# Kernel tuning notes

Measured on AMD Instinct MI355X. Metric: run time of the kernel, lower is better.

Reference implementation:

```python
import jax, jax.numpy as jnp
import numpy as np
from jax import lax

EPS = 1e-5
NBIT = 127.0  # 8-bit symmetric: 2^(8-1)-1

def ste_round(x):
    return x + lax.stop_gradient(jnp.round(x) - x)

def quant_act(x, rng_max):
    # symmetric fake-quant of activations with learned per-cluster range
    s = rng_max / NBIT
    xq = jnp.clip(ste_round(x / s), -NBIT, NBIT) * s
    return xq, s

def fold_bn(w, gamma, beta, mean, var):
    std = jnp.sqrt(var + EPS)
    scale = gamma / std
    w_f = w * scale[:, None, None, None]
    b_f = beta - mean * scale
    return w_f, b_f

def quant_weight(w):
    # per-output-channel symmetric quant
    s = jnp.max(jnp.abs(w), axis=(1, 2, 3), keepdims=True) / NBIT
    wq = jnp.clip(ste_round(w / s), -NBIT, NBIT) * s
    return wq, s.reshape(-1)

def conv(x, w, stride=1, groups=1, pad=0):
    return lax.conv_general_dilated(
        x, w, window_strides=(stride, stride),
        padding=((pad, pad), (pad, pad)),
        dimension_numbers=('NCHW', 'OIHW', 'NCHW'),
        feature_group_count=groups)

def setup_inputs() -> dict:
    key = jax.random.key(0)
    ks = jax.random.split(key, 24)
    B, Cin, H, W = 64, 96, 28, 28
    Cmid, Cout, NC = 576, 96, 4
    d = {}
    d['x'] = jax.random.normal(ks[0], (B, Cin, H, W), dtype=jnp.float32)
    # conv1: 1x1 expansion
    d['w1'] = jax.random.normal(ks[1], (Cmid, Cin, 1, 1), jnp.float32) * 0.1
    d['g1'] = jax.random.uniform(ks[2], (Cmid,), minval=0.5, maxval=1.5)
    d['b1'] = jax.random.normal(ks[3], (Cmid,)) * 0.1
    d['m1'] = jax.random.normal(ks[4], (Cmid,)) * 0.1
    d['v1'] = jax.random.uniform(ks[5], (Cmid,), minval=0.5, maxval=1.5)
    # conv2: 3x3 depthwise
    d['w2'] = jax.random.normal(ks[6], (Cmid, 1, 3, 3), jnp.float32) * 0.1
    d['g2'] = jax.random.uniform(ks[7], (Cmid,), minval=0.5, maxval=1.5)
    d['b2'] = jax.random.normal(ks[8], (Cmid,)) * 0.1
    d['m2'] = jax.random.normal(ks[9], (Cmid,)) * 0.1
    d['v2'] = jax.random.uniform(ks[10], (Cmid,), minval=0.5, maxval=1.5)
    # conv3: 1x1 projection
    d['w3'] = jax.random.normal(ks[11], (Cout, Cmid, 1, 1), jnp.float32) * 0.1
    d['g3'] = jax.random.uniform(ks[12], (Cout,), minval=0.5, maxval=1.5)
    d['b3'] = jax.random.normal(ks[13], (Cout,)) * 0.1
    d['m3'] = jax.random.normal(ks[14], (Cout,)) * 0.1
    d['v3'] = jax.random.uniform(ks[15], (Cout,), minval=0.5, maxval=1.5)
    # per-cluster learned activation ranges for the 4 QuantAct modules
    d['r0'] = jax.random.uniform(ks[16], (NC,), minval=2.0, maxval=8.0)
    d['r1'] = jax.random.uniform(ks[17], (NC,), minval=2.0, maxval=8.0)
    d['r2'] = jax.random.uniform(ks[18], (NC,), minval=2.0, maxval=8.0)
    d['r3'] = jax.random.uniform(ks[19], (NC,), minval=2.0, maxval=8.0)
    d['cluster'] = 2
    return d

def reference(x, w1, g1, b1, m1, v1, w2, g2, b2, m2, v2,
              w3, g3, b3, m3, v3, r0, r1, r2, r3, cluster):
    identity = x  # residual path (in==out, stride==1)
    # QuantAct -> conv1 (BN-folded, per-channel quant) -> ReLU6
    xq, s0 = quant_act(x, r0[cluster])
    w1f, bf1 = fold_bn(w1, g1, b1, m1, v1)
    w1q, ws1 = quant_weight(w1f)
    y = conv(xq, w1q) + bf1[None, :, None, None]
    y = jnp.clip(y, 0.0, 6.0)
    # QuantAct1 -> depthwise conv2 -> ReLU6
    yq, s1 = quant_act(y, r1[cluster])
    w2f, bf2 = fold_bn(w2, g2, b2, m2, v2)
    w2q, ws2 = quant_weight(w2f)
    y = conv(yq, w2q, stride=1, groups=w2.shape[0], pad=1) + bf2[None, :, None, None]
    y = jnp.clip(y, 0.0, 6.0)
    # QuantAct2 -> conv3 projection
    yq, s2 = quant_act(y, r2[cluster])
    w3f, bf3 = fold_bn(w3, g3, b3, m3, v3)
    w3q, ws3 = quant_weight(w3f)
    y = conv(yq, w3q) + bf3[None, :, None, None]
    # residual add, then int32 requant
    y = y + identity
    out, s3 = quant_act(y, r3[cluster])
    return out, s3
```

## Files before the change

kernel.cpp:

```cpp
#include <hip/hip_runtime.h>
#include <cstdint>
#include <cstddef>

typedef int   v4i __attribute__((ext_vector_type(4)));
typedef float v4f __attribute__((ext_vector_type(4)));
typedef unsigned int u32;

constexpr int B_   = 64;
constexpr int CIN  = 96;
constexpr int P_   = 784;
constexpr int CMID = 576;
constexpr int COUT = 96;
constexpr int NOUT = B_ * COUT * P_;
constexpr float NBITF = 127.0f;
constexpr float EPSF  = 1e-5f;

constexpr int XKD = 36;
constexpr int YKD = 144;
constexpr int XBD = 13 * XKD * 64;
constexpr int YBD = 13 * YKD * 64;

__device__ __forceinline__ int dot3(u32 a, u32 w, int acc) {
#if __has_builtin(__builtin_amdgcn_sdot4)
    return __builtin_amdgcn_sdot4((int)a, (int)w, acc, false);
#else
    return acc + (int)(signed char)(a)        * (int)(signed char)(w)
               + (int)(signed char)(a >> 8)   * (int)(signed char)(w >> 8)
               + (int)(signed char)(a >> 16)  * (int)(signed char)(w >> 16);
#endif
}

__device__ __forceinline__ void tr4(u32 S0, u32 S1, u32 S2, u32 S3, u32 O[4]) {
    u32 u01 = __builtin_amdgcn_perm(S1, S0, 0x05010400u);
    u32 u23 = __builtin_amdgcn_perm(S3, S2, 0x05010400u);
    u32 v01 = __builtin_amdgcn_perm(S1, S0, 0x07030602u);
    u32 v23 = __builtin_amdgcn_perm(S3, S2, 0x07030602u);
    O[0] = __builtin_amdgcn_perm(u23, u01, 0x05040100u);
    O[1] = __builtin_amdgcn_perm(u23, u01, 0x07060302u);
    O[2] = __builtin_amdgcn_perm(v23, v01, 0x05040100u);
    O[3] = __builtin_amdgcn_perm(v23, v01, 0x07060302u);
}

__global__ __launch_bounds__(64)
void prep_weights(const float* __restrict__ w1, const float* __restrict__ g1,
                  const float* __restrict__ b1, const float* __restrict__ m1,
                  const float* __restrict__ v1,
                  const float* __restrict__ w2, const float* __restrict__ g2,
                  const float* __restrict__ b2, const float* __restrict__ m2,
                  const float* __restrict__ v2,
                  const float* __restrict__ w3, const float* __restrict__ g3,
                  const float* __restrict__ b3, const float* __restrict__ m3,
                  const float* __restrict__ v3,
                  int8_t* __restrict__ w1qp, float* __restrict__ ws1, float* __restrict__ bf1,
                  v4i* __restrict__ w2pk, float* __restrict__ ws2, float* __restrict__ bf2,
                  int8_t* __restrict__ w3qp, float* __restrict__ ws3, float* __restrict__ bf3)
{
    int blk  = blockIdx.x;
    int lane = threadIdx.x;

    const float *w, *g, *bb, *mm, *vv;
    int oc, K, which;
    if (blk < CMID)            { which = 0; w = w1; g = g1; bb = b1; mm = m1; vv = v1; oc = blk;            K = CIN;  }
    else if (blk < 2 * CMID)   { which = 1; w = w2; g = g2; bb = b2; mm = m2; vv = v2; oc = blk - CMID;     K = 9;    }
    else                       { which = 2; w = w3; g = g3; bb = b3; mm = m3; vv = v3; oc = blk - 2 * CMID; K = CMID; }

    float scale = g[oc] / sqrtf(vv[oc] + EPSF);

    float mx = 0.f;
    for (int k = lane; k < K; k += 64)
        mx = fmaxf(mx, fabsf(w[oc * K + k] * scale));
    #pragma unroll
    for (int off = 1; off < 64; off <<= 1)
        mx = fmaxf(mx, __shfl_xor(mx, off));

    float s = mx / NBITF;

    int myq = 0;
    for (int k = lane; k < K; k += 64) {
        float wf = w[oc * K + k] * scale;
        float q  = fminf(fmaxf(rintf(wf / s), -127.f), 127.f);
        if (which == 0)      w1qp[oc * 144 + k] = (int8_t)q;
        else if (which == 1) myq = (int)q;
        else                 w3qp[oc * 592 + k] = (int8_t)q;
    }
    if (which == 0 && lane < 12)
        ((u32*)(w1qp + oc * 144))[24 + lane] = 0u;
    if (which == 1) {
        u32 qq[9];
        #pragma unroll
        for (int t = 0; t < 9; t++) qq[t] = (u32)__shfl(myq, t, 64) & 0xffu;
        if (lane == 0) {
            v4i pk;
            pk[0] = (int)(qq[0] | (qq[1] << 8) | (qq[2] << 16));
            pk[1] = (int)(qq[3] | (qq[4] << 8) | (qq[5] << 16));
            pk[2] = (int)(qq[6] | (qq[7] << 8) | (qq[8] << 16));
            pk[3] = 0;
            w2pk[oc] = pk;
        }
    }
    if (lane == 0) {
        float bf = bb[oc] - mm[oc] * scale;
        if (which == 0)      { ws1[oc] = s; bf1[oc] = bf; }
        else if (which == 1) { ws2[oc] = s; bf2[oc] = bf; }
        else                 { ws3[oc] = s; bf3[oc] = bf; }
    }
}

__global__ __launch_bounds__(256)
void quant_x(const float* __restrict__ x, const float* __restrict__ r0,
             const int* __restrict__ cluster, u32* __restrict__ x8t)
{
    __shared__ u32 T[112 * 37];

    int tid = threadIdx.x, pt0 = blockIdx.x, b = blockIdx.y;
    float inv_s0 = NBITF / r0[cluster[0]];

    for (int i = tid; i < 112 * 12; i += 256) {
        int row = i / 12, cpad = i - row * 12;
        T[row * 37 + 24 + cpad] = 0u;
    }
    for (int u = tid; u < 24 * 28; u += 256) {
        int pq = u % 28, icq = u / 28;
        int pxb = pt0 * 112 + pq * 4;
        int q[4][4];
        #pragma unroll
        for (int j = 0; j < 4; j++) {
            v4f xv = *(const v4f*)(x + ((size_t)b * CIN + icq * 4 + j) * P_ + pxb);
            #pragma unroll
            for (int i = 0; i < 4; i++)
                q[j][i] = (int)fminf(fmaxf(rintf(xv[i] * inv_s0), -127.f), 127.f);
        }
        #pragma unroll
        for (int i = 0; i < 4; i++) {
            u32 t0 = __builtin_amdgcn_perm((u32)q[1][i], (u32)q[0][i], 0x00000400u);
            u32 t1 = __builtin_amdgcn_perm((u32)q[3][i], (u32)q[2][i], 0x00000400u);
            T[(pq * 4 + i) * 37 + icq] = __builtin_amdgcn_perm(t1, t0, 0x05040100u);
        }
    }
    __syncthreads();
    u32* gb = x8t + (size_t)b * XBD;
    for (int i = tid; i < XKD * 112; i += 256) {
        int icq = i / 112, pxo = i - icq * 112;
        int px = pt0 * 112 + pxo;
        gb[(((px >> 6) * XKD) + icq) * 64 + (px & 63)] = T[pxo * 37 + icq];
    }
}

__global__ __launch_bounds__(256)
void conv12(const u32* __restrict__ x8t, const int8_t* __restrict__ w1qp,
            const float* __restrict__ ws1, const float* __restrict__ bf1,
            const v4i* __restrict__ w2pk, const float* __restrict__ ws2,
            const float* __restrict__ bf2,
            const float* __restrict__ r0, const float* __restrict__ r1,
            const float* __restrict__ r2, const int* __restrict__ cluster,
            u32* __restrict__ y2qT)
{
    __shared__ u32 AY[6912];
    __shared__ u32 PB[5488];

    int tid = threadIdx.x;
    int b   = blockIdx.y;
    int mt  = blockIdx.x / 14, rt = blockIdx.x - mt * 14;
    int oc0 = mt * 192;
    int R0  = rt * 2;
    int W0  = (R0 - 1) * 28;

    int   c      = cluster[0];
    float s0     = r0[c] / NBITF;
    float s1     = r1[c] / NBITF;
    float inv_s1 = NBITF / r1[c];
    float inv_s2 = NBITF / r2[c];
    float u1     = fminf(rintf(6.f * inv_s1), 127.f);
    float u2     = fminf(rintf(6.f * inv_s2), 127.f);

    {
        const v4i* gs = (const v4i*)(w1qp + (size_t)oc0 * 144);
        v4i* ld = (v4i*)AY;
        for (int i = tid; i < 192 * 9; i += 256) ld[i] = gs[i];
    }
    __syncthreads();

    int lane = tid & 63, wv = tid >> 6;
    int n = lane & 15, q4 = lane >> 4;

    const u32* xb = x8t + (size_t)b * XBD;
    int pbase[7];
    #pragma unroll
    for (int j = 0; j < 7; j++) {
        int px = W0 + j * 16 + n;
        px = min(max(px, 0), P_ - 1);
        pbase[j] = ((px >> 6) * XKD) * 64 + (px & 63);
    }

    v4i acc[3][7];
    #pragma unroll
    for (int i = 0; i < 3; i++)
        #pragma unroll
        for (int j = 0; j < 7; j++) acc[i][j] = (v4i){0, 0, 0, 0};

    const v4i* Af = (const v4i*)AY;
    #pragma unroll
    for (int ks = 0; ks < 2; ks++) {
        int k0 = ks * 16 + q4 * 4;
        v4i bfr[7], afr[3];
        #pragma unroll
        for (int j = 0; j < 7; j++) {
            u32 d0 = xb[pbase[j] + (k0 + 0) * 64];
            u32 d1 = xb[pbase[j] + (k0 + 1) * 64];
            u32 d2 = xb[pbase[j] + (k0 + 2) * 64];
            u32 d3 = xb[pbase[j] + (k0 + 3) * 64];
            bfr[j] = (v4i){(int)d0, (int)d1, (int)d2, (int)d3};
        }
        #pragma unroll
        for (int i = 0; i < 3; i++)
            afr[i] = Af[(wv * 48 + i * 16 + n) * 9 + ks * 4 + q4];
        #pragma unroll
        for (int i = 0; i < 3; i++)
            #pragma unroll
            for (int j = 0; j < 7; j++)
                acc[i][j] = __builtin_amdgcn_mfma_i32_16x16x64_i8(afr[i], bfr[j], acc[i][j], 0, 0, 0);
    }

    float sA[3][4], bA[3][4];
    #pragma unroll
    for (int i = 0; i < 3; i++)
        #pragma unroll
        for (int r = 0; r < 4; r++) {
            int oc = oc0 + wv * 48 + i * 16 + q4 * 4 + r;
            sA[i][r] = s0 * ws1[oc] * inv_s1;
            bA[i][r] = bf1[oc] * inv_s1;
        }
    #pragma unroll
    for (int i = 0; i < 3; i++) {
        int chq = wv * 12 + i * 4 + q4;
        #pragma unroll
        for (int j = 0; j < 7; j++) {
            int pxl = j * 16 + n;
            bool valid = (unsigned)(W0 + pxl) < (unsigned)P_;
            u32 pk = 0;
            #pragma unroll
            for (int r = 0; r < 4; r++) {
                float t = fmaf((float)acc[i][j][r], sA[i][r], bA[i][r]);
                t = fminf(fmaxf(rintf(t), 0.f), u1);
                pk |= ((u32)(int)t) << (8 * r);
            }
            PB[pxl * 49 + chq] = valid ? pk : 0u;
        }
    }
    __syncthreads();

    for (int u = tid; u < 1536; u += 256) {
        int cc = u & 7, rowl = (u >> 3) & 3, chq = u >> 5;
        u32 S[4];
        #pragma unroll
        for (int k = 0; k < 4; k++) {
            int col = 4 * cc - 1 + k;
            S[k] = ((unsigned)col < 28u) ? PB[(rowl * 28 + col) * 49 + chq] : 0u;
        }
        u32 O[4];
        tr4(S[0], S[1], S[2], S[3], O);
        int bse = chq * 132 + rowl * 8 + cc;
        #pragma unroll
        for (int r = 0; r < 4; r++) AY[bse + r * 33] = O[r];
    }
    __syncthreads();

    for (int u = tid; u < 2688; u += 256) {
        int xq = u % 7;
        int t2 = u / 7;
        int orow = t2 & 1;
        int chl  = t2 >> 1;
        int chg  = oc0 + chl;

        v4i wpk = w2pk[chg];
        int base = chl * 33 + orow * 8;
        int a0 = 0, a1 = 0, a2 = 0, a3 = 0;
        #pragma unroll
        for (int dr = 0; dr < 3; dr++) {
            u32 d0 = AY[base + dr * 8 + xq];
            u32 d1 = AY[base + dr * 8 + xq + 1];
            u32 pk = (u32)((dr == 0) ? wpk[0] : (dr == 1) ? wpk[1] : wpk[2]);
            a0 = dot3(d0, pk, a0);
            a1 = dot3(__builtin_amdgcn_alignbyte(d1, d0, 1), pk, a1);
            a2 = dot3(__builtin_amdgcn_alignbyte(d1, d0, 2), pk, a2);
            a3 = dot3(__builtin_amdgcn_alignbyte(d1, d0, 3), pk, a3);
        }
        float sc = s1 * ws2[chg] * inv_s2;
        float bb = bf2[chg] * inv_s2;
        int aa[4] = {a0, a1, a2, a3};
        u32 pk2 = 0;
        #pragma unroll
        for (int i = 0; i < 4; i++) {
            float t = fmaf((float)aa[i], sc, bb);
            t = fminf(fmaxf(rintf(t), 0.f), u2);
            pk2 |= ((u32)(int)t) << (8 * i);
        }
        PB[chl * 15 + orow * 7 + xq] = pk2;
    }
    __syncthreads();

    u32* yb = y2qT + (size_t)b * YBD;
    int kdw0 = mt * 48;
    for (int u = tid; u < 672; u += 256) {
        int pxq = u % 14, chq = u / 14;
        int orow = pxq / 7, xq = pxq - orow * 7;
        u32 S[4];
        #pragma unroll
        for (int r = 0; r < 4; r++) S[r] = PB[(chq * 4 + r) * 15 + pxq];
        u32 O[4];
        tr4(S[0], S[1], S[2], S[3], O);
        #pragma unroll
        for (int k = 0; k < 4; k++) {
            int gpx = (R0 + orow) * 28 + xq * 4 + k;
            yb[((gpx >> 6) * YKD + kdw0 + chq) * 64 + (gpx & 63)] = O[k];
        }
    }
}

__global__ __launch_bounds__(256)
void conv3_kernel(const u32* __restrict__ y2qT, const int8_t* __restrict__ w3qp,
                  const float* __restrict__ ws3, const float* __restrict__ bf3,
                  const float* __restrict__ x, const float* __restrict__ r2,
                  const float* __restrict__ r3, const int* __restrict__ cluster,
                  float* __restrict__ out)
{
    __shared__ u32 Ash[96 * 148];

    int tid = threadIdx.x, b = blockIdx.y, pt = blockIdx.x;

    int   c      = cluster[0];
    float s2     = r2[c] / NBITF;
    float s3     = r3[c] / NBITF;
    float inv_s3 = NBITF / r3[c];

    {
        const v4i* gs = (const v4i*)w3qp;
        v4i* ld = (v4i*)Ash;
        for (int i = tid; i < 96 * 37; i += 256) ld[i] = gs[i];
    }
    __syncthreads();

    int lane = tid & 63, wv = tid >> 6;
    int n = lane & 15, q4 = lane >> 4;
    int pxl = wv * 16 + n;

    const u32* yb = y2qT + (size_t)b * YBD + (size_t)pt * (YKD * 64) + pxl;
    const v4i* Af = (const v4i*)Ash;

    v4i acc[6];
    #pragma unroll
    for (int i = 0; i < 6; i++) acc[i] = (v4i){0, 0, 0, 0};

    #pragma unroll
    for (int ks = 0; ks < 9; ks++) {
        int k0 = ks * 16 + q4 * 4;
        u32 d0 = yb[(k0 + 0) * 64];
        u32 d1 = yb[(k0 + 1) * 64];
        u32 d2 = yb[(k0 + 2) * 64];
        u32 d3 = yb[(k0 + 3) * 64];
        v4i bfr = (v4i){(int)d0, (int)d1, (int)d2, (int)d3};
        #pragma unroll
        for (int i = 0; i < 6; i++) {
            v4i afr = Af[(i * 16 + n) * 37 + ks * 4 + q4];
            acc[i] = __builtin_amdgcn_mfma_i32_16x16x64_i8(afr, bfr, acc[i], 0, 0, 0);
        }
    }

    int px = pt * 64 + pxl;
    if (px < P_) {
        #pragma unroll
        for (int i = 0; i < 6; i++)
            #pragma unroll
            for (int r = 0; r < 4; r++) {
                int oc = i * 16 + q4 * 4 + r;
                size_t gi = ((size_t)b * COUT + oc) * P_ + px;
                float v  = (float)acc[i][r] * (s2 * ws3[oc]) + bf3[oc] + x[gi];
                float qv = fminf(fmaxf(rintf(v * inv_s3), -127.f), 127.f);
                out[gi] = qv * s3;
            }
    }
    if (pt == 0 && b == 0 && tid == 0)
        out[NOUT] = s3;
}

extern "C" void kernel_launch(void* const* d_in, const int* in_sizes, int n_in,
                              void* d_out, int out_size, void* d_ws, size_t ws_size,
                              hipStream_t stream)
{
    const float* x  = (const float*)d_in[0];
    const float* w1 = (const float*)d_in[1];
    const float* g1 = (const float*)d_in[2];
    const float* b1 = (const float*)d_in[3];
    const float* m1 = (const float*)d_in[4];
    const float* v1 = (const float*)d_in[5];
    const float* w2 = (const float*)d_in[6];
    const float* g2 = (const float*)d_in[7];
    const float* b2 = (const float*)d_in[8];
    const float* m2 = (const float*)d_in[9];
    const float* v2 = (const float*)d_in[10];
    const float* w3 = (const float*)d_in[11];
    const float* g3 = (const float*)d_in[12];
    const float* b3 = (const float*)d_in[13];
    const float* m3 = (const float*)d_in[14];
    const float* v3 = (const float*)d_in[15];
    const float* r0 = (const float*)d_in[16];
    const float* r1 = (const float*)d_in[17];
    const float* r2 = (const float*)d_in[18];
    const float* r3 = (const float*)d_in[19];
    const int*   cl = (const int*)d_in[20];

    float* out = (float*)d_out;

    char*  ws  = (char*)d_ws;
    size_t off = 0;
    auto carve = [&](size_t bytes) {
        size_t cur = off;
        off = (off + bytes + 255) & ~(size_t)255;
        return (void*)(ws + cur);
    };
    int8_t* w1qp = (int8_t*)carve((size_t)CMID * 144);
    float*  ws1  = (float*)carve(CMID * 4);
    float*  bf1  = (float*)carve(CMID * 4);
    v4i*    w2pk = (v4i*)carve((size_t)CMID * 16);
    float*  ws2  = (float*)carve(CMID * 4);
    float*  bf2  = (float*)carve(CMID * 4);
    int8_t* w3qp = (int8_t*)carve((size_t)COUT * 592);
    float*  ws3  = (float*)carve(COUT * 4);
    float*  bf3  = (float*)carve(COUT * 4);
    u32*    x8t  = (u32*)carve((size_t)B_ * XBD * 4);
    u32*    y2qT = (u32*)carve((size_t)B_ * YBD * 4);
    (void)ws_size; (void)in_sizes; (void)n_in; (void)out_size;

    prep_weights<<<dim3(2 * CMID + COUT), dim3(64), 0, stream>>>(
        w1, g1, b1, m1, v1, w2, g2, b2, m2, v2, w3, g3, b3, m3, v3,
        w1qp, ws1, bf1, w2pk, ws2, bf2, w3qp, ws3, bf3);

    quant_x<<<dim3(7, B_), dim3(256), 0, stream>>>(x, r0, cl, x8t);

    conv12<<<dim3(42, B_), dim3(256), 0, stream>>>(
        x8t, w1qp, ws1, bf1, w2pk, ws2, bf2, r0, r1, r2, cl, y2qT);

    conv3_kernel<<<dim3(13, B_), dim3(256), 0, stream>>>(
        y2qT, w3qp, ws3, bf3, x, r2, r3, cl, out);
}
```

Before: 191.0 us.

## Split fused conv1+depthwise kernel into separate conv1, depthwise, conv3 kernels

The fused conv1+depthwise kernel is split into three kernels: an MFMA 1x1 expansion that writes packed int8 rows in channel-major layout, a per-row depthwise kernel that reads them from global memory, and a projection kernel that transposes the activations into LDS instead of the weights. Rounding and clamping now use the magic-number float trick on integer bits. The change drops the halo recomputation and the shared-memory staging of the fused kernel. In exchange the full 576-channel intermediate makes an extra round trip through global memory, and the x8t buffer is aliased onto y2px.

After: 187.7 us. No clear change (-1.7%).

```diff
diff --git a/kernel.cpp b/kernel.cpp
--- a/kernel.cpp
+++ b/kernel.cpp
@@ -14,11 +14,11 @@
 constexpr int NOUT = B_ * COUT * P_;
 constexpr float NBITF = 127.0f;
 constexpr float EPSF  = 1e-5f;
+constexpr float MAGICF = 12582912.0f;
+constexpr int   BIASI  = 0x4B400000;
 
 constexpr int XKD = 36;
-constexpr int YKD = 144;
 constexpr int XBD = 13 * XKD * 64;
-constexpr int YBD = 13 * YKD * 64;
 
 __device__ __forceinline__ int dot3(u32 a, u32 w, int acc) {
 #if __has_builtin(__builtin_amdgcn_sdot4)
@@ -39,6 +39,12 @@
     O[1] = __builtin_amdgcn_perm(u23, u01, 0x07060302u);
     O[2] = __builtin_amdgcn_perm(v23, v01, 0x05040100u);
     O[3] = __builtin_amdgcn_perm(v23, v01, 0x07060302u);
+}
+
+__device__ __forceinline__ u32 pack4(u32 t0, u32 t1, u32 t2, u32 t3) {
+    u32 p01 = __builtin_amdgcn_perm(t1, t0, 0x05010400u);
+    u32 p23 = __builtin_amdgcn_perm(t3, t2, 0x05010400u);
+    return __builtin_amdgcn_perm(p23, p01, 0x05040100u);
 }
 
 __global__ __launch_bounds__(64)
@@ -147,196 +153,175 @@
 }
 
 __global__ __launch_bounds__(256)
-void conv12(const u32* __restrict__ x8t, const int8_t* __restrict__ w1qp,
+void conv1s(const u32* __restrict__ x8t, const int8_t* __restrict__ w1qp,
             const float* __restrict__ ws1, const float* __restrict__ bf1,
-            const v4i* __restrict__ w2pk, const float* __restrict__ ws2,
-            const float* __restrict__ bf2,
             const float* __restrict__ r0, const float* __restrict__ r1,
-            const float* __restrict__ r2, const int* __restrict__ cluster,
-            u32* __restrict__ y2qT)
-{
-    __shared__ u32 AY[6912];
-    __shared__ u32 PB[5488];
-
-    int tid = threadIdx.x;
-    int b   = blockIdx.y;
-    int mt  = blockIdx.x / 14, rt = blockIdx.x - mt * 14;
-    int oc0 = mt * 192;
-    int R0  = rt * 2;
-    int W0  = (R0 - 1) * 28;
+            const int* __restrict__ cluster, u32* __restrict__ y1px)
+{
+    int tid = threadIdx.x, b = blockIdx.y;
+    int mt = blockIdx.x % 3, pt = blockIdx.x / 3;
+    int p0 = pt * 64;
+    int lane = tid & 63, wv = tid >> 6;
+    int n = lane & 15, q4 = lane >> 4;
+    int ocw = mt * 192 + wv * 48;
 
     int   c      = cluster[0];
     float s0     = r0[c] / NBITF;
-    float s1     = r1[c] / NBITF;
     float inv_s1 = NBITF / r1[c];
-    float inv_s2 = NBITF / r2[c];
-    float u1     = fminf(rintf(6.f * inv_s1), 127.f);
-    float u2     = fminf(rintf(6.f * inv_s2), 127.f);
-
-    {
-        const v4i* gs = (const v4i*)(w1qp + (size_t)oc0 * 144);
-        v4i* ld = (v4i*)AY;
-        for (int i = tid; i < 192 * 9; i += 256) ld[i] = gs[i];
-    }
-    __syncthreads();
-
-    int lane = tid & 63, wv = tid >> 6;
-    int n = lane & 15, q4 = lane >> 4;
+    int   u1i    = (int)fminf(rintf(6.f * inv_s1), 127.f);
 
     const u32* xb = x8t + (size_t)b * XBD;
-    int pbase[7];
-    #pragma unroll
-    for (int j = 0; j < 7; j++) {
-        int px = W0 + j * 16 + n;
-        px = min(max(px, 0), P_ - 1);
-        pbase[j] = ((px >> 6) * XKD) * 64 + (px & 63);
-    }
-
-    v4i acc[3][7];
-    #pragma unroll
-    for (int i = 0; i < 3; i++)
-        #pragma unroll
-        for (int j = 0; j < 7; j++) acc[i][j] = (v4i){0, 0, 0, 0};
-
-    const v4i* Af = (const v4i*)AY;
+    int abase[4];
+    #pragma unroll
+    for (int jm = 0; jm < 4; jm++) {
+        int px = p0 + 16 * jm + n;
+        px = min(px, P_ - 1);
+        abase[jm] = ((px >> 6) * XKD) * 64 + (px & 63);
+    }
+
+    v4i acc[3][4];
+    #pragma unroll
+    for (int jn = 0; jn < 3; jn++)
+        #pragma unroll
+        for (int jm = 0; jm < 4; jm++) acc[jn][jm] = (v4i){0, 0, 0, 0};
+
+    const v4i* w4 = (const v4i*)w1qp;
     #pragma unroll
     for (int ks = 0; ks < 2; ks++) {
-        int k0 = ks * 16 + q4 * 4;
-        v4i bfr[7], afr[3];
-        #pragma unroll
-        for (int j = 0; j < 7; j++) {
-            u32 d0 = xb[pbase[j] + (k0 + 0) * 64];
-            u32 d1 = xb[pbase[j] + (k0 + 1) * 64];
-            u32 d2 = xb[pbase[j] + (k0 + 2) * 64];
-            u32 d3 = xb[pbase[j] + (k0 + 3) * 64];
-            bfr[j] = (v4i){(int)d0, (int)d1, (int)d2, (int)d3};
-        }
-        #pragma unroll
-        for (int i = 0; i < 3; i++)
-            afr[i] = Af[(wv * 48 + i * 16 + n) * 9 + ks * 4 + q4];
-        #pragma unroll
-        for (int i = 0; i < 3; i++)
+        v4i bfr[3], afr[4];
+        #pragma unroll
+        for (int jn = 0; jn < 3; jn++) {
+            int oc = ocw + 16 * jn + n;
+            bfr[jn] = w4[oc * 9 + ks * 4 + q4];
+        }
+        #pragma unroll
+        for (int jm = 0; jm < 4; jm++) {
+            int kb = (16 * ks + 4 * q4) * 64;
+            u32 d0 = xb[abase[jm] + kb];
+            u32 d1 = xb[abase[jm] + kb + 64];
+            u32 d2 = xb[abase[jm] + kb + 128];
+            u32 d3 = xb[abase[jm] + kb + 192];
+            afr[jm] = (v4i){(int)d0, (int)d1, (int)d2, (int)d3};
+        }
+        #pragma unroll
+        for (int jn = 0; jn < 3; jn++)
             #pragma unroll
-            for (int j = 0; j < 7; j++)
-                acc[i][j] = __builtin_amdgcn_mfma_i32_16x16x64_i8(afr[i], bfr[j], acc[i][j], 0, 0, 0);
-    }
-
-    float sA[3][4], bA[3][4];
-    #pragma unroll
-    for (int i = 0; i < 3; i++)
-        #pragma unroll
-        for (int r = 0; r < 4; r++) {
-            int oc = oc0 + wv * 48 + i * 16 + q4 * 4 + r;
-            sA[i][r] = s0 * ws1[oc] * inv_s1;
-            bA[i][r] = bf1[oc] * inv_s1;
-        }
-    #pragma unroll
-    for (int i = 0; i < 3; i++) {
-        int chq = wv * 12 + i * 4 + q4;
-        #pragma unroll
-        for (int j = 0; j < 7; j++) {
-            int pxl = j * 16 + n;
-            bool valid = (unsigned)(W0 + pxl) < (unsigned)P_;
-            u32 pk = 0;
+            for (int jm = 0; jm < 4; jm++)
+                acc[jn][jm] = __builtin_amdgcn_mfma_i32_16x16x64_i8(afr[jm], bfr[jn], acc[jn][jm], 0, 0, 0);
+    }
+
+    #pragma unroll
+    for (int jn = 0; jn < 3; jn++) {
+        int   oc  = ocw + 16 * jn + n;
+        float scv = s0 * ws1[oc] * inv_s1;
+        float bbv = bf1[oc] * inv_s1;
+        size_t rowbase = (size_t)(b * CMID + oc) * 196 + (p0 >> 2);
+        #pragma unroll
+        for (int jm = 0; jm < 4; jm++) {
+            int quad = p0 + 16 * jm + 4 * q4;
+            u32 t[4];
             #pragma unroll
             for (int r = 0; r < 4; r++) {
-                float t = fmaf((float)acc[i][j][r], sA[i][r], bA[i][r]);
-                t = fminf(fmaxf(rintf(t), 0.f), u1);
-                pk |= ((u32)(int)t) << (8 * r);
+                float f = fmaf((float)acc[jn][jm][r], scv, bbv) + MAGICF;
+                int v = __float_as_int(f);
+                t[r] = (u32)min(max(v, BIASI), BIASI + u1i);
             }
-            PB[pxl * 49 + chq] = valid ? pk : 0u;
-        }
-    }
-    __syncthreads();
-
-    for (int u = tid; u < 1536; u += 256) {
-        int cc = u & 7, rowl = (u >> 3) & 3, chq = u >> 5;
-        u32 S[4];
-        #pragma unroll
-        for (int k = 0; k < 4; k++) {
-            int col = 4 * cc - 1 + k;
-            S[k] = ((unsigned)col < 28u) ? PB[(rowl * 28 + col) * 49 + chq] : 0u;
-        }
-        u32 O[4];
-        tr4(S[0], S[1], S[2], S[3], O);
-        int bse = chq * 132 + rowl * 8 + cc;
-        #pragma unroll
-        for (int r = 0; r < 4; r++) AY[bse + r * 33] = O[r];
-    }
-    __syncthreads();
-
-    for (int u = tid; u < 2688; u += 256) {
-        int xq = u % 7;
-        int t2 = u / 7;
-        int orow = t2 & 1;
-        int chl  = t2 >> 1;
-        int chg  = oc0 + chl;
-
-        v4i wpk = w2pk[chg];
-        int base = chl * 33 + orow * 8;
+            if (quad < P_)
+                y1px[rowbase + 4 * jm + q4] = pack4(t[0], t[1], t[2], t[3]);
+        }
+    }
+}
+
+__global__ __launch_bounds__(256)
+void conv2s(const u32* __restrict__ y1px, const v4i* __restrict__ w2pk,
+            const float* __restrict__ ws2, const float* __restrict__ bf2,
+            const float* __restrict__ r1, const float* __restrict__ r2,
+            const int* __restrict__ cluster, u32* __restrict__ y2px)
+{
+    int gid = blockIdx.x * 256 + threadIdx.x;
+    int r  = gid % 28;
+    int t  = gid / 28;
+    int ch = t % CMID;
+    int b  = t / CMID;
+
+    int   c      = cluster[0];
+    float s1     = r1[c] / NBITF;
+    float inv_s2 = NBITF / r2[c];
+    int   u2i    = (int)fminf(rintf(6.f * inv_s2), 127.f);
+
+    const u32* base = y1px + (size_t)(b * CMID + ch) * 196;
+    u32 R[3][7];
+    #pragma unroll
+    for (int dr = 0; dr < 3; dr++) {
+        int rr = r + dr - 1;
+        bool ok = (unsigned)rr < 28u;
+        #pragma unroll
+        for (int j = 0; j < 7; j++)
+            R[dr][j] = ok ? base[rr * 7 + j] : 0u;
+    }
+
+    v4i wpk = w2pk[ch];
+    u32 pk0 = (u32)wpk[0], pk1 = (u32)wpk[1], pk2 = (u32)wpk[2];
+    float scv = s1 * ws2[ch] * inv_s2;
+    float bbv = bf2[ch] * inv_s2;
+
+    u32* orow = y2px + (size_t)(b * CMID + ch) * 196 + r * 7;
+    #pragma unroll
+    for (int j = 0; j < 7; j++) {
         int a0 = 0, a1 = 0, a2 = 0, a3 = 0;
         #pragma unroll
         for (int dr = 0; dr < 3; dr++) {
-            u32 d0 = AY[base + dr * 8 + xq];
-            u32 d1 = AY[base + dr * 8 + xq + 1];
-            u32 pk = (u32)((dr == 0) ? wpk[0] : (dr == 1) ? wpk[1] : wpk[2]);
-            a0 = dot3(d0, pk, a0);
-            a1 = dot3(__builtin_amdgcn_alignbyte(d1, d0, 1), pk, a1);
-            a2 = dot3(__builtin_amdgcn_alignbyte(d1, d0, 2), pk, a2);
-            a3 = dot3(__builtin_amdgcn_alignbyte(d1, d0, 3), pk, a3);
-        }
-        float sc = s1 * ws2[chg] * inv_s2;
-        float bb = bf2[chg] * inv_s2;
+            u32 D   = R[dr][j];
+            u32 Dm1 = (j > 0) ? R[dr][j - 1] : 0u;
+            u32 Dp1 = (j < 6) ? R[dr][j + 1] : 0u;
+            u32 pk  = (dr == 0) ? pk0 : (dr == 1) ? pk1 : pk2;
+            a0 = dot3(__builtin_amdgcn_alignbyte(D, Dm1, 3), pk, a0);
+            a1 = dot3(D, pk, a1);
+            a2 = dot3(__builtin_amdgcn_alignbyte(Dp1, D, 1), pk, a2);
+            a3 = dot3(__builtin_amdgcn_alignbyte(Dp1, D, 2), pk, a3);
+        }
         int aa[4] = {a0, a1, a2, a3};
-        u32 pk2 = 0;
+        u32 tq[4];
         #pragma unroll
         for (int i = 0; i < 4; i++) {
-            float t = fmaf((float)aa[i], sc, bb);
-            t = fminf(fmaxf(rintf(t), 0.f), u2);
-            pk2 |= ((u32)(int)t) << (8 * i);
-        }
-        PB[chl * 15 + orow * 7 + xq] = pk2;
-    }
-    __syncthreads();
-
-    u32* yb = y2qT + (size_t)b * YBD;
-    int kdw0 = mt * 48;
-    for (int u = tid; u < 672; u += 256) {
-        int pxq = u % 14, chq = u / 14;
-        int orow = pxq / 7, xq = pxq - orow * 7;
-        u32 S[4];
-        #pragma unroll
-        for (int r = 0; r < 4; r++) S[r] = PB[(chq * 4 + r) * 15 + pxq];
-        u32 O[4];
-        tr4(S[0], S[1], S[2], S[3], O);
-        #pragma unroll
-        for (int k = 0; k < 4; k++) {
-            int gpx = (R0 + orow) * 28 + xq * 4 + k;
-            yb[((gpx >> 6) * YKD + kdw0 + chq) * 64 + (gpx & 63)] = O[k];
-        }
+            float f = fmaf((float)aa[i], scv, bbv) + MAGICF;
+            int v = __float_as_int(f);
+            tq[i] = (u32)min(max(v, BIASI), BIASI + u2i);
+        }
+        orow[j] = pack4(tq[0], tq[1], tq[2], tq[3]);
     }
 }
 
 __global__ __launch_bounds__(256)
-void conv3_kernel(const u32* __restrict__ y2qT, const int8_t* __restrict__ w3qp,
-                  const float* __restrict__ ws3, const float* __restrict__ bf3,
-                  const float* __restrict__ x, const float* __restrict__ r2,
-                  const float* __restrict__ r3, const int* __restrict__ cluster,
-                  float* __restrict__ out)
-{
-    __shared__ u32 Ash[96 * 148];
+void conv3s(const u32* __restrict__ y2px, const int8_t* __restrict__ w3qp,
+            const float* __restrict__ ws3, const float* __restrict__ bf3,
+            const float* __restrict__ x, const float* __restrict__ r2,
+            const float* __restrict__ r3, const int* __restrict__ cluster,
+            float* __restrict__ out)
+{
+    __shared__ u32 Bsh[144 * 67];
 
     int tid = threadIdx.x, b = blockIdx.y, pt = blockIdx.x;
+    int p0d = pt * 16;
 
     int   c      = cluster[0];
     float s2     = r2[c] / NBITF;
     float s3     = r3[c] / NBITF;
     float inv_s3 = NBITF / r3[c];
 
-    {
-        const v4i* gs = (const v4i*)w3qp;
-        v4i* ld = (v4i*)Ash;
-        for (int i = tid; i < 96 * 37; i += 256) ld[i] = gs[i];
+    for (int u = tid; u < 2304; u += 256) {
+        int pxq = u & 15, chq = u >> 4;
+        u32 S[4];
+        #pragma unroll
+        for (int r = 0; r < 4; r++) {
+            int col = min(p0d + pxq, 195);
+            S[r] = y2px[(size_t)(b * CMID + 4 * chq + r) * 196 + col];
+        }
+        u32 O[4];
+        tr4(S[0], S[1], S[2], S[3], O);
+        #pragma unroll
+        for (int k = 0; k < 4; k++)
+            Bsh[chq * 67 + 4 * pxq + k] = O[k];
     }
     __syncthreads();
 
@@ -344,24 +329,21 @@
     int n = lane & 15, q4 = lane >> 4;
     int pxl = wv * 16 + n;
 
-    const u32* yb = y2qT + (size_t)b * YBD + (size_t)pt * (YKD * 64) + pxl;
-    const v4i* Af = (const v4i*)Ash;
-
     v4i acc[6];
     #pragma unroll
     for (int i = 0; i < 6; i++) acc[i] = (v4i){0, 0, 0, 0};
 
     #pragma unroll
     for (int ks = 0; ks < 9; ks++) {
-        int k0 = ks * 16 + q4 * 4;
-        u32 d0 = yb[(k0 + 0) * 64];
-        u32 d1 = yb[(k0 + 1) * 64];
-        u32 d2 = yb[(k0 + 2) * 64];
-        u32 d3 = yb[(k0 + 3) * 64];
-        v4i bfr = (v4i){(int)d0, (int)d1, (int)d2, (int)d3};
+        int kr = 16 * ks + 4 * q4;
+        u32 b0 = Bsh[(kr + 0) * 67 + pxl];
+        u32 b1 = Bsh[(kr + 1) * 67 + pxl];
+        u32 b2 = Bsh[(kr + 2) * 67 + pxl];
+        u32 b3 = Bsh[(kr + 3) * 67 + pxl];
+        v4i bfr = (v4i){(int)b0, (int)b1, (int)b2, (int)b3};
         #pragma unroll
         for (int i = 0; i < 6; i++) {
-            v4i afr = Af[(i * 16 + n) * 37 + ks * 4 + q4];
+            v4i afr = *(const v4i*)(w3qp + (size_t)(i * 16 + n) * 592 + ks * 64 + q4 * 16);
             acc[i] = __builtin_amdgcn_mfma_i32_16x16x64_i8(afr, bfr, acc[i], 0, 0, 0);
         }
     }
@@ -369,15 +351,17 @@
     int px = pt * 64 + pxl;
     if (px < P_) {
         #pragma unroll
-        for (int i = 0; i < 6; i++)
+        for (int i = 0; i < 6; i++) {
             #pragma unroll
             for (int r = 0; r < 4; r++) {
                 int oc = i * 16 + q4 * 4 + r;
-                size_t gi = ((size_t)b * COUT + oc) * P_ + px;
+                size_t gi = (size_t)(b * COUT + oc) * P_ + px;
                 float v  = (float)acc[i][r] * (s2 * ws3[oc]) + bf3[oc] + x[gi];
-                float qv = fminf(fmaxf(rintf(v * inv_s3), -127.f), 127.f);
-                out[gi] = qv * s3;
+                float f  = fmaf(v, inv_s3, MAGICF);
+                int lvl  = min(max(__float_as_int(f) - BIASI, -127), 127);
+                out[gi]  = (float)lvl * s3;
             }
+        }
     }
     if (pt == 0 && b == 0 && tid == 0)
         out[NOUT] = s3;
@@ -427,8 +411,9 @@
     int8_t* w3qp = (int8_t*)carve((size_t)COUT * 592);
     float*  ws3  = (float*)carve(COUT * 4);
     float*  bf3  = (float*)carve(COUT * 4);
-    u32*    x8t  = (u32*)carve((size_t)B_ * XBD * 4);
-    u32*    y2qT = (u32*)carve((size_t)B_ * YBD * 4);
+    u32*    y1px = (u32*)carve((size_t)B_ * CMID * 196 * 4);
+    u32*    y2px = (u32*)carve((size_t)B_ * CMID * 196 * 4);
+    u32*    x8t  = y2px;
     (void)ws_size; (void)in_sizes; (void)n_in; (void)out_size;
 
     prep_weights<<<dim3(2 * CMID + COUT), dim3(64), 0, stream>>>(
@@ -437,9 +422,12 @@
 
     quant_x<<<dim3(7, B_), dim3(256), 0, stream>>>(x, r0, cl, x8t);
 
-    conv12<<<dim3(42, B_), dim3(256), 0, stream>>>(
-        x8t, w1qp, ws1, bf1, w2pk, ws2, bf2, r0, r1, r2, cl, y2qT);
-
-    conv3_kernel<<<dim3(13, B_), dim3(256), 0, stream>>>(
-        y2qT, w3qp, ws3, bf3, x, r2, r3, cl, out);
-}
+    conv1s<<<dim3(39, B_), dim3(256), 0, stream>>>(
+        x8t, w1qp, ws1, bf1, r0, r1, cl, y1px);
+
+    conv2s<<<dim3((B_ * CMID * 28) / 256), dim3(256), 0, stream>>>(
+        y1px, w2pk, ws2, bf2, r1, r2, cl, y2px);
+
+    conv3s<<<dim3(13, B_), dim3(256), 0, stream>>>(
+        y2px, w3qp, ws3, bf3, x, r2, r3, cl, out);
+}
```
